# Performance work log

Hardware: AMD Instinct MI355X
Metric: run time of the kernel (lower is better)

The kernel has to match this reference:

```python
import jax, jax.numpy as jnp
import numpy as np

N, D, E, K = 8192, 1024, 16, 2
CAP = 1024  # capacity_per_expert


def setup_inputs() -> dict:
    key = jax.random.key(0)
    k1, k2, k3 = jax.random.split(key, 3)
    return {
        "moe_inp": jax.random.normal(k1, (N, D), dtype=jnp.float32),
        "gate_w": jax.random.normal(k2, (D, E), dtype=jnp.float32) * 0.02,
        "gate_b": jnp.zeros((E,), dtype=jnp.float32),
        "expert_w": jax.random.normal(k3, (E, D, D), dtype=jnp.float32) * 0.02,
        "expert_b": jnp.zeros((E, D), dtype=jnp.float32),
    }


def _capacity_keep_mask(expert_id, slot_score, num_experts, capacity):
    """For each flattened (token, k) slot assigned to an expert, keep only the
    `capacity` slots with the highest token score (gate_score.max over k),
    matching the argsort-based drop in _fmoe_limited_global_forward."""
    nslots = expert_id.shape[0]
    # sort slots by (expert asc, score desc)
    order = jnp.lexsort((-slot_score, expert_id))
    counts = jnp.bincount(expert_id, length=num_experts)
    starts = jnp.concatenate([jnp.zeros((1,), counts.dtype), jnp.cumsum(counts)[:-1]])
    pos_in_expert = jnp.arange(nslots) - starts[expert_id[order]]
    keep_sorted = pos_in_expert < capacity
    return jnp.zeros((nslots,), dtype=bool).at[order].set(keep_sorted)


def reference(moe_inp, gate_w, gate_b, expert_w, expert_b):
    n, d = moe_inp.shape
    e = expert_w.shape[0]
    # NaiveGate: linear -> top-k -> softmax over the k selected logits
    logits = moe_inp @ gate_w + gate_b                       # [N, E]
    top_v, top_i = jax.lax.top_k(logits, K)                  # [N, K]
    gate_score = jax.nn.softmax(top_v, axis=-1)              # [N, K]

    expert_id = top_i.reshape(-1)                            # [N*K]
    token_id = jnp.arange(n * K) // K                        # [N*K]
    mask_scores = gate_score.max(axis=-1)                    # [N] per-token score
    slot_score = mask_scores[token_id]                       # [N*K]

    keep = _capacity_keep_mask(expert_id, slot_score, e, CAP).reshape(n, K)

    # expert forward: FMoELinear y = x @ W_e^T + b_e (dense over experts, then gather)
    all_out = jnp.einsum('nd,efd->nef', moe_inp, expert_w) + expert_b  # [N, E, D]
    y = jnp.take_along_axis(all_out, top_i[:, :, None], axis=1)        # [N, K, D]
    # dropped (over-capacity) slots pass the scattered input through unchanged
    y = jnp.where(keep[:, :, None], y, moe_inp[:, None, :])
    # combine: bmm(gate_score [N,1,K], y [N,K,D]) -> [N, D]
    return jnp.einsum('nk,nkd->nd', gate_score, y)
```

## Files before the change

kernel.cpp:

```cpp
#include <hip/hip_runtime.h>
#include <hip/hip_bf16.h>
#include <math.h>

#define N_TOK 8192
#define DIM   1024
#define NEXP  16
#define TOPK  2
#define CAPE  1024
#define NSLOT (N_TOK*TOPK)

typedef __attribute__((ext_vector_type(8))) short     short8;
typedef __attribute__((ext_vector_type(4))) float     floatx4;
typedef __attribute__((ext_vector_type(4))) unsigned short ushort4v;

__device__ __forceinline__ unsigned short f2bf(float f) {
    unsigned u = __float_as_uint(f);
    u += 0x7FFFu + ((u >> 16) & 1u);
    return (unsigned short)(u >> 16);
}

#define GLOAD_LDS16(g, l) __builtin_amdgcn_global_load_lds( \
    (const __attribute__((address_space(1))) unsigned int*)(g), \
    (__attribute__((address_space(3))) unsigned int*)(l), 16, 0, 0)

#define RAW_BARRIER() asm volatile("s_barrier" ::: "memory")

__global__ void gwt_kernel(const float* __restrict__ gw, float* __restrict__ gwT) {
    int i = blockIdx.x * 256 + threadIdx.x;
    if (i >= DIM * NEXP) return;
    int d = i >> 4, e = i & 15;
    gwT[e * DIM + d] = gw[i];
}

__global__ __launch_bounds__(256) void gate_kernel(
        const float* __restrict__ x,
        const float* __restrict__ gwT,
        const float* __restrict__ gb,
        int* __restrict__ slot_expert,
        unsigned long long* __restrict__ slot_key,
        float* __restrict__ slot_gate,
        unsigned short* __restrict__ Xb) {
    const int t    = blockIdx.x * 4 + (threadIdx.x >> 6);
    const int lane = threadIdx.x & 63;

    const floatx4* xr = (const floatx4*)(x + (size_t)t * DIM);
    ushort4v* Xb4 = (ushort4v*)Xb + (size_t)t * 256;
    floatx4 xv[4];
#pragma unroll
    for (int i = 0; i < 4; i++) {
        xv[i] = xr[lane + i * 64];
        ushort4v o;
        o[0] = f2bf(xv[i][0]); o[1] = f2bf(xv[i][1]);
        o[2] = f2bf(xv[i][2]); o[3] = f2bf(xv[i][3]);
        Xb4[lane + i * 64] = o;
    }

    float acc[NEXP];
#pragma unroll
    for (int e = 0; e < NEXP; e++) {
        const floatx4* wr = (const floatx4*)(gwT + (size_t)e * DIM);
        float a = 0.f;
#pragma unroll
        for (int i = 0; i < 4; i++) {
            floatx4 w = wr[lane + i * 64];
            a += xv[i][0]*w[0] + xv[i][1]*w[1] + xv[i][2]*w[2] + xv[i][3]*w[3];
        }
        acc[e] = a;
    }
#pragma unroll
    for (int off = 32; off > 0; off >>= 1) {
#pragma unroll
        for (int e = 0; e < NEXP; e++) acc[e] += __shfl_down(acc[e], off, 64);
    }
    if (lane == 0) {
        float v0 = -1e30f; int i0 = 0;
#pragma unroll
        for (int e = 0; e < NEXP; e++) {
            float v = acc[e] + gb[e];
            acc[e] = v;
            if (v > v0) { v0 = v; i0 = e; }
        }
        float v1 = -1e30f; int i1 = 0;
#pragma unroll
        for (int e = 0; e < NEXP; e++) {
            if (e != i0 && acc[e] > v1) { v1 = acc[e]; i1 = e; }
        }
        float e1 = expf(v1 - v0);
        float den = 1.f + e1;
        float g0 = 1.f / den;
        float g1 = e1 / den;
        unsigned sb = __float_as_uint(g0);
        int s0 = 2 * t, s1 = 2 * t + 1;
        slot_expert[s0] = i0; slot_expert[s1] = i1;
        slot_gate[s0]   = g0; slot_gate[s1]   = g1;
        unsigned long long hi = ((unsigned long long)sb) << 32;
        slot_key[s0] = hi | (unsigned)(0xFFFFFFFFu - (unsigned)s0);
        slot_key[s1] = hi | (unsigned)(0xFFFFFFFFu - (unsigned)s1);
    }
}

__global__ __launch_bounds__(256) void bucket_kernel(
        const int* __restrict__ slot_expert,
        const unsigned long long* __restrict__ slot_key,
        int* __restrict__ counts,
        unsigned long long* __restrict__ buckets) {
    __shared__ int lcnt[NEXP];
    __shared__ int lbase[NEXP];
    const int tid = threadIdx.x;
    const int s = blockIdx.x * 256 + tid;
    if (tid < NEXP) lcnt[tid] = 0;
    __syncthreads();
    const int e = slot_expert[s];
    const unsigned long long key = slot_key[s];
    const int lpos = atomicAdd(&lcnt[e], 1);
    __syncthreads();
    if (tid < NEXP) lbase[tid] = lcnt[tid] ? atomicAdd(&counts[tid], lcnt[tid]) : 0;
    __syncthreads();
    buckets[(size_t)e * NSLOT + lbase[e] + lpos] = key;
}

__global__ __launch_bounds__(256) void keep_wave_kernel(
        const int* __restrict__ slot_expert,
        const unsigned long long* __restrict__ slot_key,
        const int* __restrict__ counts,
        const unsigned long long* __restrict__ buckets,
        int* __restrict__ slot_keep) {
    const int wv   = threadIdx.x >> 6;
    const int lane = threadIdx.x & 63;
    const int s    = blockIdx.x * 4 + wv;
    const int e    = slot_expert[s];
    const int c    = counts[e];
    int kp = 1;
    if (c > CAPE) {
        const unsigned long long k = slot_key[s];
        const unsigned long long* bk = buckets + (size_t)e * NSLOT;
        int rank = 0;
        for (int i = lane; i < c; i += 64) rank += (bk[i] > k) ? 1 : 0;
#pragma unroll
        for (int off = 32; off > 0; off >>= 1) rank += __shfl_down(rank, off, 64);
        kp = (__shfl(rank, 0, 64) < CAPE) ? 1 : 0;
    }
    if (lane == 0) slot_keep[s] = kp;
}

__global__ __launch_bounds__(256) void compact_kernel(
        const int* __restrict__ slot_expert,
        const int* __restrict__ slot_keep,
        int* __restrict__ ecount,
        int* __restrict__ elist,
        int* __restrict__ slot_pos) {
    __shared__ int lcnt[NEXP];
    __shared__ int lbase[NEXP];
    const int tid = threadIdx.x;
    const int s = blockIdx.x * 256 + tid;
    if (tid < NEXP) lcnt[tid] = 0;
    __syncthreads();
    const int e  = slot_expert[s];
    const int kp = slot_keep[s];
    int lpos = 0;
    if (kp) lpos = atomicAdd(&lcnt[e], 1);
    __syncthreads();
    if (tid < NEXP) lbase[tid] = lcnt[tid] ? atomicAdd(&ecount[tid], lcnt[tid]) : 0;
    __syncthreads();
    if (kp) {
        int p = lbase[e] + lpos;
        elist[e * CAPE + p] = s;
        if (slot_pos) slot_pos[s] = e * CAPE + p;
    }
}

__global__ void base_kernel(const float* __restrict__ x,
                            const int* __restrict__ keep,
                            const float* __restrict__ gate,
                            float* __restrict__ out) {
    int i = blockIdx.x * blockDim.x + threadIdx.x;
    int t = i >> 8;
    float c = 0.f;
    if (!keep[2 * t])     c += gate[2 * t];
    if (!keep[2 * t + 1]) c += gate[2 * t + 1];
    floatx4 v = ((const floatx4*)x)[i];
    ((floatx4*)out)[i] = v * c;
}

__global__ void cvt_kernel(const float* __restrict__ src,
                           unsigned short* __restrict__ dst, int n4) {
    int i = blockIdx.x * blockDim.x + threadIdx.x;
    if (i >= n4) return;
    floatx4 v = ((const floatx4*)src)[i];
    ushort4v o;
    o[0] = f2bf(v[0]); o[1] = f2bf(v[1]); o[2] = f2bf(v[2]); o[3] = f2bf(v[3]);
    ((ushort4v*)dst)[i] = o;
}

template <bool STORE_YS>
__global__ __launch_bounds__(512, 4)
void moe_gemm(const unsigned short* __restrict__ Xb,
              const unsigned short* __restrict__ Wb,
              const float* __restrict__ eb,
              const int* __restrict__ elist,
              const int* __restrict__ ecount,
              const float* __restrict__ slot_gate,
              float* __restrict__ ys,
              float* __restrict__ out) {
    __shared__ unsigned short As[2][256 * 32];
    __shared__ unsigned short Bs[2][128 * 32];

    const int e  = blockIdx.z;
    const int ne = ecount[e];
    const int m0 = blockIdx.y * 256;
    if (m0 >= ne) return;
    const int n0   = blockIdx.x * 128;
    const int tid  = threadIdx.x;
    const int wv   = tid >> 6;
    const int lane = tid & 63;
    const int q    = lane >> 4;
    const int l15  = lane & 15;
    const int wm   = (wv >> 1) * 64;
    const int wn   = (wv & 1) * 64;

    const int srow = wv * 16 + (lane >> 2);
    const int jsrc = (lane & 3) ^ ((lane >> 3) & 3);
    const unsigned short* gA0;
    const unsigned short* gA1;
    {
        int m = m0 + srow;
        int slot = elist[e * CAPE + (m < ne ? m : 0)];
        gA0 = Xb + (size_t)(slot >> 1) * DIM + jsrc * 8;
        m = m0 + 128 + srow;
        slot = elist[e * CAPE + (m < ne ? m : 0)];
        gA1 = Xb + (size_t)(slot >> 1) * DIM + jsrc * 8;
    }
    const unsigned short* gB0 =
        Wb + (size_t)e * DIM * DIM + (size_t)(n0 + srow) * DIM + jsrc * 8;

#define STAGE(b, k0) do { \
    GLOAD_LDS16(gA0 + (k0), &As[b][(wv * 16) * 32]); \
    GLOAD_LDS16(gA1 + (k0), &As[b][(128 + wv * 16) * 32]); \
    GLOAD_LDS16(gB0 + (k0), &Bs[b][(wv * 16) * 32]); } while (0)

    STAGE(0, 0);
    STAGE(1, 32);

    const int swz  = (q ^ ((l15 >> 1) & 3)) * 8;
    const int aoff = (wm + l15) * 32 + swz;
    const int boff = (wn + l15) * 32 + swz;

    floatx4 acc[4][4] = {};
    short8 a[4], b[4];

    for (int t = 0; t < 32; t++) {
        const int cur = t & 1;
        if (t == 31) { asm volatile("s_waitcnt vmcnt(0)" ::: "memory"); }
        else         { asm volatile("s_waitcnt vmcnt(3)" ::: "memory"); }
        __builtin_amdgcn_sched_barrier(0);
        RAW_BARRIER();

        const unsigned short* A_ = &As[cur][0];
        const unsigned short* B_ = &Bs[cur][0];
#pragma unroll
        for (int fi = 0; fi < 4; fi++) a[fi] = *(const short8*)(A_ + aoff + fi * 512);
#pragma unroll
        for (int fj = 0; fj < 4; fj++) b[fj] = *(const short8*)(B_ + boff + fj * 512);

        __builtin_amdgcn_s_setprio(1);
#pragma unroll
        for (int fi = 0; fi < 4; fi++)
#pragma unroll
            for (int fj = 0; fj < 4; fj++)
                acc[fi][fj] = __builtin_amdgcn_mfma_f32_16x16x32_bf16(
                    a[fi], b[fj], acc[fi][fj], 0, 0, 0);
        __builtin_amdgcn_s_setprio(0);
        RAW_BARRIER();

        if (t + 2 < 32) STAGE(cur, (t + 2) * 32);
    }
#undef STAGE

    float ebv[4];
#pragma unroll
    for (int fj = 0; fj < 4; fj++)
        ebv[fj] = eb[e * DIM + n0 + wn + fj * 16 + l15];
#pragma unroll
    for (int fi = 0; fi < 4; fi++) {
        const int mrow = m0 + wm + fi * 16 + q * 4;
#pragma unroll
        for (int r = 0; r < 4; r++) {
            int m = mrow + r;
            if (m >= ne) continue;
            if (STORE_YS) {
                float* yrow = ys + ((size_t)e * CAPE + m) * DIM + n0 + wn;
#pragma unroll
                for (int fj = 0; fj < 4; fj++)
                    yrow[fj * 16 + l15] = acc[fi][fj][r] + ebv[fj];
            } else {
                int slot = elist[e * CAPE + m];
                int tok  = slot >> 1;
                float g  = slot_gate[slot];
                float* orow = out + (size_t)tok * DIM + n0 + wn;
#pragma unroll
                for (int fj = 0; fj < 4; fj++)
                    atomicAdd(orow + fj * 16 + l15, g * (acc[fi][fj][r] + ebv[fj]));
            }
        }
    }
}

__global__ void combine_kernel(const float* __restrict__ x,
                               const float* __restrict__ ys,
                               const int* __restrict__ keep,
                               const int* __restrict__ pos,
                               const float* __restrict__ gate,
                               float* __restrict__ out) {
    int i = blockIdx.x * 256 + threadIdx.x;
    int t = i >> 8;
    int c = i & 255;
    int s0 = 2 * t, s1 = s0 + 1;
    floatx4 xv = ((const floatx4*)x)[i];
    float g0 = gate[s0], g1 = gate[s1];
    floatx4 r;
    if (keep[s0]) {
        floatx4 y0 = ((const floatx4*)ys)[((size_t)pos[s0] << 8) + c];
        r = y0 * g0;
    } else r = xv * g0;
    if (keep[s1]) {
        floatx4 y1 = ((const floatx4*)ys)[((size_t)pos[s1] << 8) + c];
        r += y1 * g1;
    } else r += xv * g1;
    ((floatx4*)out)[i] = r;
}

extern "C" void kernel_launch(void* const* d_in, const int* in_sizes, int n_in,
                              void* d_out, int out_size, void* d_ws, size_t ws_size,
                              hipStream_t stream) {
    const float* x  = (const float*)d_in[0];
    const float* gw = (const float*)d_in[1];
    const float* gb = (const float*)d_in[2];
    const float* ew = (const float*)d_in[3];
    const float* eb = (const float*)d_in[4];
    float* out = (float*)d_out;

    char* ws = (char*)d_ws;
    int* counts      = (int*)(ws + 0);
    int* ecount      = (int*)(ws + 64);
    int* slot_expert = (int*)(ws + 256);
    int* slot_keep   = (int*)(ws + 65792);
    float* slot_gate = (float*)(ws + 131328);
    unsigned long long* slot_key = (unsigned long long*)(ws + 196864);
    unsigned long long* buckets  = (unsigned long long*)(ws + 327936);
    int* elist       = (int*)(ws + 2425088);
    float* gwT       = (float*)(ws + 2490624);
    unsigned short* Xb = (unsigned short*)(ws + 2556160);
    unsigned short* Wb = (unsigned short*)(ws + 19333376);
    int* slot_pos    = (int*)(ws + 52887808);
    int* ecount2     = (int*)(ws + 52953088);
    float* ys        = (float*)(ws + 52953344);
    const size_t WS_NEED_YS = 52953344ull + (size_t)NEXP * CAPE * DIM * 4;

    const bool ys_path = (ws_size >= WS_NEED_YS);
    (void)ecount2;

    hipMemsetAsync(ws, 0, 256, stream);

    gwt_kernel <<<64, 256, 0, stream>>>(gw, gwT);
    gate_kernel<<<N_TOK / 4, 256, 0, stream>>>(x, gwT, gb, slot_expert, slot_key,
                                               slot_gate, Xb);
    bucket_kernel<<<NSLOT / 256, 256, 0, stream>>>(slot_expert, slot_key, counts, buckets);
    keep_wave_kernel<<<NSLOT / 4, 256, 0, stream>>>(slot_expert, slot_key, counts,
                                                    buckets, slot_keep);
    compact_kernel<<<NSLOT / 256, 256, 0, stream>>>(slot_expert, slot_keep, ecount, elist,
                                                    ys_path ? slot_pos : nullptr);
    cvt_kernel<<<(NEXP * DIM * DIM / 4) / 256, 256, 0, stream>>>(ew, Wb, NEXP * DIM * DIM / 4);

    if (ys_path) {
        moe_gemm<true><<<dim3(8, 4, 16), 512, 0, stream>>>(Xb, Wb, eb, elist, ecount,
                                                           slot_gate, ys, out);
        combine_kernel<<<N_TOK, 256, 0, stream>>>(x, ys, slot_keep, slot_pos,
                                                  slot_gate, out);
    } else {
        base_kernel<<<(N_TOK * DIM / 4) / 256, 256, 0, stream>>>(x, slot_keep,
                                                                 slot_gate, out);
        moe_gemm<false><<<dim3(8, 4, 16), 512, 0, stream>>>(Xb, Wb, eb, elist, ecount,
                                                            slot_gate, nullptr, out);
    }
}
```

Measured before the change: 243.8 us.

## Split MoE GEMM into per-k passes writing output directly, drop ys buffer

```diff
diff --git a/kernel.cpp b/kernel.cpp
--- a/kernel.cpp
+++ b/kernel.cpp
@@ -120,11 +120,14 @@
 }
 
 __global__ __launch_bounds__(256) void keep_wave_kernel(
+        const float* __restrict__ x,
         const int* __restrict__ slot_expert,
         const unsigned long long* __restrict__ slot_key,
         const int* __restrict__ counts,
         const unsigned long long* __restrict__ buckets,
-        int* __restrict__ slot_keep) {
+        const float* __restrict__ slot_gate,
+        int* __restrict__ slot_keep,
+        float* __restrict__ out) {
     const int wv   = threadIdx.x >> 6;
     const int lane = threadIdx.x & 63;
     const int s    = blockIdx.x * 4 + wv;
@@ -141,45 +144,49 @@
         kp = (__shfl(rank, 0, 64) < CAPE) ? 1 : 0;
     }
     if (lane == 0) slot_keep[s] = kp;
+    if (!kp && !(s & 1)) {
+        const int t = s >> 1;
+        const float g = slot_gate[s];
+        const floatx4* xr = (const floatx4*)(x + (size_t)t * DIM);
+        floatx4* orow = (floatx4*)(out + (size_t)t * DIM);
+#pragma unroll
+        for (int i = 0; i < 4; i++) orow[lane + i * 64] = xr[lane + i * 64] * g;
+    }
 }
 
 __global__ __launch_bounds__(256) void compact_kernel(
         const int* __restrict__ slot_expert,
         const int* __restrict__ slot_keep,
-        int* __restrict__ ecount,
-        int* __restrict__ elist,
-        int* __restrict__ slot_pos) {
-    __shared__ int lcnt[NEXP];
-    __shared__ int lbase[NEXP];
+        int* __restrict__ ecntP,
+        int* __restrict__ ndrop,
+        int* __restrict__ elist0,
+        int* __restrict__ elist1,
+        int* __restrict__ droplist) {
+    __shared__ int lcnt[2 * NEXP];
+    __shared__ int lbase[2 * NEXP];
+    __shared__ int ldc, ldbase;
     const int tid = threadIdx.x;
     const int s = blockIdx.x * 256 + tid;
-    if (tid < NEXP) lcnt[tid] = 0;
+    if (tid < 2 * NEXP) lcnt[tid] = 0;
+    if (tid == 2 * NEXP) ldc = 0;
     __syncthreads();
     const int e  = slot_expert[s];
+    const int p  = s & 1;
     const int kp = slot_keep[s];
-    int lpos = 0;
-    if (kp) lpos = atomicAdd(&lcnt[e], 1);
-    __syncthreads();
-    if (tid < NEXP) lbase[tid] = lcnt[tid] ? atomicAdd(&ecount[tid], lcnt[tid]) : 0;
+    const int idx = p * NEXP + e;
+    int lpos = 0, dpos = 0;
+    if (kp) lpos = atomicAdd(&lcnt[idx], 1);
+    else if (p) dpos = atomicAdd(&ldc, 1);
+    __syncthreads();
+    if (tid < 2 * NEXP) lbase[tid] = lcnt[tid] ? atomicAdd(&ecntP[tid], lcnt[tid]) : 0;
+    if (tid == 2 * NEXP) ldbase = ldc ? atomicAdd(ndrop, ldc) : 0;
     __syncthreads();
     if (kp) {
-        int p = lbase[e] + lpos;
-        elist[e * CAPE + p] = s;
-        if (slot_pos) slot_pos[s] = e * CAPE + p;
-    }
-}
-
-__global__ void base_kernel(const float* __restrict__ x,
-                            const int* __restrict__ keep,
-                            const float* __restrict__ gate,
-                            float* __restrict__ out) {
-    int i = blockIdx.x * blockDim.x + threadIdx.x;
-    int t = i >> 8;
-    float c = 0.f;
-    if (!keep[2 * t])     c += gate[2 * t];
-    if (!keep[2 * t + 1]) c += gate[2 * t + 1];
-    floatx4 v = ((const floatx4*)x)[i];
-    ((floatx4*)out)[i] = v * c;
+        int* el = p ? elist1 : elist0;
+        el[e * CAPE + lbase[idx] + lpos] = s;
+    } else if (p) {
+        droplist[ldbase + dpos] = s;
+    }
 }
 
 __global__ void cvt_kernel(const float* __restrict__ src,
@@ -192,21 +199,41 @@
     ((ushort4v*)dst)[i] = o;
 }
 
-template <bool STORE_YS>
+__global__ __launch_bounds__(256) void drop_add_kernel(
+        const float* __restrict__ x,
+        const float* __restrict__ slot_gate,
+        const int* __restrict__ droplist,
+        const int* __restrict__ ndrop,
+        float* __restrict__ out) {
+    const int wv   = blockIdx.x * 4 + (threadIdx.x >> 6);
+    const int lane = threadIdx.x & 63;
+    const int nw   = gridDim.x * 4;
+    const int nd   = *ndrop;
+    for (int i = wv; i < nd; i += nw) {
+        const int s = droplist[i];
+        const int t = s >> 1;
+        const float g = slot_gate[s];
+        const floatx4* xr = (const floatx4*)(x + (size_t)t * DIM);
+        floatx4* orow = (floatx4*)(out + (size_t)t * DIM);
+#pragma unroll
+        for (int j = 0; j < 4; j++) orow[lane + j * 64] += xr[lane + j * 64] * g;
+    }
+}
+
+template <int PASS>
 __global__ __launch_bounds__(512, 4)
 void moe_gemm(const unsigned short* __restrict__ Xb,
               const unsigned short* __restrict__ Wb,
               const float* __restrict__ eb,
               const int* __restrict__ elist,
-              const int* __restrict__ ecount,
+              const int* __restrict__ ecnt,
               const float* __restrict__ slot_gate,
-              float* __restrict__ ys,
               float* __restrict__ out) {
     __shared__ unsigned short As[2][256 * 32];
     __shared__ unsigned short Bs[2][128 * 32];
 
     const int e  = blockIdx.z;
-    const int ne = ecount[e];
+    const int ne = ecnt[e];
     const int m0 = blockIdx.y * 256;
     if (m0 >= ne) return;
     const int n0   = blockIdx.x * 128;
@@ -287,46 +314,18 @@
         for (int r = 0; r < 4; r++) {
             int m = mrow + r;
             if (m >= ne) continue;
-            if (STORE_YS) {
-                float* yrow = ys + ((size_t)e * CAPE + m) * DIM + n0 + wn;
-#pragma unroll
-                for (int fj = 0; fj < 4; fj++)
-                    yrow[fj * 16 + l15] = acc[fi][fj][r] + ebv[fj];
-            } else {
-                int slot = elist[e * CAPE + m];
-                int tok  = slot >> 1;
-                float g  = slot_gate[slot];
-                float* orow = out + (size_t)tok * DIM + n0 + wn;
-#pragma unroll
-                for (int fj = 0; fj < 4; fj++)
-                    atomicAdd(orow + fj * 16 + l15, g * (acc[fi][fj][r] + ebv[fj]));
+            int slot = elist[e * CAPE + m];
+            int tok  = slot >> 1;
+            float g  = slot_gate[slot];
+            float* orow = out + (size_t)tok * DIM + n0 + wn;
+#pragma unroll
+            for (int fj = 0; fj < 4; fj++) {
+                float v = g * (acc[fi][fj][r] + ebv[fj]);
+                if (PASS == 0) orow[fj * 16 + l15] = v;
+                else           orow[fj * 16 + l15] += v;
             }
         }
     }
-}
-
-__global__ void combine_kernel(const float* __restrict__ x,
-                               const float* __restrict__ ys,
-                               const int* __restrict__ keep,
-                               const int* __restrict__ pos,
-                               const float* __restrict__ gate,
-                               float* __restrict__ out) {
-    int i = blockIdx.x * 256 + threadIdx.x;
-    int t = i >> 8;
-    int c = i & 255;
-    int s0 = 2 * t, s1 = s0 + 1;
-    floatx4 xv = ((const floatx4*)x)[i];
-    float g0 = gate[s0], g1 = gate[s1];
-    floatx4 r;
-    if (keep[s0]) {
-        floatx4 y0 = ((const floatx4*)ys)[((size_t)pos[s0] << 8) + c];
-        r = y0 * g0;
-    } else r = xv * g0;
-    if (keep[s1]) {
-        floatx4 y1 = ((const floatx4*)ys)[((size_t)pos[s1] << 8) + c];
-        r += y1 * g1;
-    } else r += xv * g1;
-    ((floatx4*)out)[i] = r;
 }
 
 extern "C" void kernel_launch(void* const* d_in, const int* in_sizes, int n_in,
@@ -341,23 +340,19 @@
 
     char* ws = (char*)d_ws;
     int* counts      = (int*)(ws + 0);
-    int* ecount      = (int*)(ws + 64);
+    int* ecntP       = (int*)(ws + 64);
+    int* ndrop       = (int*)(ws + 192);
     int* slot_expert = (int*)(ws + 256);
     int* slot_keep   = (int*)(ws + 65792);
     float* slot_gate = (float*)(ws + 131328);
     unsigned long long* slot_key = (unsigned long long*)(ws + 196864);
     unsigned long long* buckets  = (unsigned long long*)(ws + 327936);
-    int* elist       = (int*)(ws + 2425088);
+    int* droplist    = (int*)(ws + 327936);
+    int* elist0      = (int*)(ws + 2425088);
     float* gwT       = (float*)(ws + 2490624);
     unsigned short* Xb = (unsigned short*)(ws + 2556160);
     unsigned short* Wb = (unsigned short*)(ws + 19333376);
-    int* slot_pos    = (int*)(ws + 52887808);
-    int* ecount2     = (int*)(ws + 52953088);
-    float* ys        = (float*)(ws + 52953344);
-    const size_t WS_NEED_YS = 52953344ull + (size_t)NEXP * CAPE * DIM * 4;
-
-    const bool ys_path = (ws_size >= WS_NEED_YS);
-    (void)ecount2;
+    int* elist1      = (int*)(ws + 52887808);
 
     hipMemsetAsync(ws, 0, 256, stream);
 
@@ -365,21 +360,15 @@
     gate_kernel<<<N_TOK / 4, 256, 0, stream>>>(x, gwT, gb, slot_expert, slot_key,
                                                slot_gate, Xb);
     bucket_kernel<<<NSLOT / 256, 256, 0, stream>>>(slot_expert, slot_key, counts, buckets);
-    keep_wave_kernel<<<NSLOT / 4, 256, 0, stream>>>(slot_expert, slot_key, counts,
-                                                    buckets, slot_keep);
-    compact_kernel<<<NSLOT / 256, 256, 0, stream>>>(slot_expert, slot_keep, ecount, elist,
-                                                    ys_path ? slot_pos : nullptr);
+    keep_wave_kernel<<<NSLOT / 4, 256, 0, stream>>>(x, slot_expert, slot_key, counts,
+                                                    buckets, slot_gate, slot_keep, out);
+    compact_kernel<<<NSLOT / 256, 256, 0, stream>>>(slot_expert, slot_keep, ecntP, ndrop,
+                                                    elist0, elist1, droplist);
     cvt_kernel<<<(NEXP * DIM * DIM / 4) / 256, 256, 0, stream>>>(ew, Wb, NEXP * DIM * DIM / 4);
 
-    if (ys_path) {
-        moe_gemm<true><<<dim3(8, 4, 16), 512, 0, stream>>>(Xb, Wb, eb, elist, ecount,
-                                                           slot_gate, ys, out);
-        combine_kernel<<<N_TOK, 256, 0, stream>>>(x, ys, slot_keep, slot_pos,
-                                                  slot_gate, out);
-    } else {
-        base_kernel<<<(N_TOK * DIM / 4) / 256, 256, 0, stream>>>(x, slot_keep,
-                                                                 slot_gate, out);
-        moe_gemm<false><<<dim3(8, 4, 16), 512, 0, stream>>>(Xb, Wb, eb, elist, ecount,
-                                                            slot_gate, nullptr, out);
-    }
-}
+    moe_gemm<0><<<dim3(8, 4, 16), 512, 0, stream>>>(Xb, Wb, eb, elist0, ecntP,
+                                                    slot_gate, out);
+    drop_add_kernel<<<64, 256, 0, stream>>>(x, slot_gate, droplist, ndrop, out);
+    moe_gemm<1><<<dim3(8, 4, 16), 512, 0, stream>>>(Xb, Wb, eb, elist1, ecntP + NEXP,
+                                                    slot_gate, out);
+}
```

Result: slower. 273.4 us (+12.1%).

## Fuse expert weight bf16 conversion into GEMM B-tile staging via registers

Applied to the files above, without the earlier changes.

```diff
diff --git a/kernel.cpp b/kernel.cpp
--- a/kernel.cpp
+++ b/kernel.cpp
@@ -182,20 +182,10 @@
     ((floatx4*)out)[i] = v * c;
 }
 
-__global__ void cvt_kernel(const float* __restrict__ src,
-                           unsigned short* __restrict__ dst, int n4) {
-    int i = blockIdx.x * blockDim.x + threadIdx.x;
-    if (i >= n4) return;
-    floatx4 v = ((const floatx4*)src)[i];
-    ushort4v o;
-    o[0] = f2bf(v[0]); o[1] = f2bf(v[1]); o[2] = f2bf(v[2]); o[3] = f2bf(v[3]);
-    ((ushort4v*)dst)[i] = o;
-}
-
 template <bool STORE_YS>
 __global__ __launch_bounds__(512, 4)
 void moe_gemm(const unsigned short* __restrict__ Xb,
-              const unsigned short* __restrict__ Wb,
+              const float* __restrict__ ew,
               const float* __restrict__ eb,
               const int* __restrict__ elist,
               const int* __restrict__ ecount,
@@ -230,16 +220,36 @@
         slot = elist[e * CAPE + (m < ne ? m : 0)];
         gA1 = Xb + (size_t)(slot >> 1) * DIM + jsrc * 8;
     }
-    const unsigned short* gB0 =
-        Wb + (size_t)e * DIM * DIM + (size_t)(n0 + srow) * DIM + jsrc * 8;
-
-#define STAGE(b, k0) do { \
+
+    const int brow = tid >> 2;
+    const int bj   = tid & 3;
+    const float* gBsrc =
+        ew + (size_t)e * DIM * DIM + (size_t)(n0 + brow) * DIM + bj * 8;
+    const int bdst = brow * 32 + (bj ^ ((brow >> 1) & 3)) * 8;
+
+#define STAGE_A(b, k0) do { \
     GLOAD_LDS16(gA0 + (k0), &As[b][(wv * 16) * 32]); \
-    GLOAD_LDS16(gA1 + (k0), &As[b][(128 + wv * 16) * 32]); \
-    GLOAD_LDS16(gB0 + (k0), &Bs[b][(wv * 16) * 32]); } while (0)
-
-    STAGE(0, 0);
-    STAGE(1, 32);
+    GLOAD_LDS16(gA1 + (k0), &As[b][(128 + wv * 16) * 32]); } while (0)
+
+    floatx4 bv0, bv1;
+#define LOADB(k0) do { bv0 = *(const floatx4*)(gBsrc + (k0)); \
+                       bv1 = *(const floatx4*)(gBsrc + (k0) + 4); } while (0)
+#define WRITEB(b) do { short8 t_; \
+    t_[0] = (short)f2bf(bv0[0]); t_[1] = (short)f2bf(bv0[1]); \
+    t_[2] = (short)f2bf(bv0[2]); t_[3] = (short)f2bf(bv0[3]); \
+    t_[4] = (short)f2bf(bv1[0]); t_[5] = (short)f2bf(bv1[1]); \
+    t_[6] = (short)f2bf(bv1[2]); t_[7] = (short)f2bf(bv1[3]); \
+    *(short8*)&Bs[b][bdst] = t_; } while (0)
+
+    LOADB(0);
+    STAGE_A(0, 0);
+    STAGE_A(1, 32);
+    asm volatile("s_waitcnt vmcnt(4)" ::: "memory");
+    __builtin_amdgcn_sched_barrier(0);
+    WRITEB(0);
+    LOADB(32);
+    asm volatile("s_waitcnt vmcnt(4)" ::: "memory");
+    __builtin_amdgcn_sched_barrier(0);
 
     const int swz  = (q ^ ((l15 >> 1) & 3)) * 8;
     const int aoff = (wm + l15) * 32 + swz;
@@ -250,8 +260,7 @@
 
     for (int t = 0; t < 32; t++) {
         const int cur = t & 1;
-        if (t == 31) { asm volatile("s_waitcnt vmcnt(0)" ::: "memory"); }
-        else         { asm volatile("s_waitcnt vmcnt(3)" ::: "memory"); }
+        asm volatile("s_waitcnt lgkmcnt(0)" ::: "memory");
         __builtin_amdgcn_sched_barrier(0);
         RAW_BARRIER();
 
@@ -272,9 +281,21 @@
         __builtin_amdgcn_s_setprio(0);
         RAW_BARRIER();
 
-        if (t + 2 < 32) STAGE(cur, (t + 2) * 32);
-    }
-#undef STAGE
+        if (t + 2 < 32) {
+            STAGE_A(cur, (t + 2) * 32);
+            asm volatile("s_waitcnt vmcnt(2)" ::: "memory");
+        } else {
+            asm volatile("s_waitcnt vmcnt(0)" ::: "memory");
+        }
+        __builtin_amdgcn_sched_barrier(0);
+        if (t + 1 < 32) {
+            WRITEB(cur ^ 1);
+            if (t + 2 < 32) LOADB((t + 2) * 32);
+        }
+    }
+#undef STAGE_A
+#undef LOADB
+#undef WRITEB
 
     float ebv[4];
 #pragma unroll
@@ -315,14 +336,16 @@
     int t = i >> 8;
     int c = i & 255;
     int s0 = 2 * t, s1 = s0 + 1;
-    floatx4 xv = ((const floatx4*)x)[i];
+    int k0 = keep[s0], k1 = keep[s1];
     float g0 = gate[s0], g1 = gate[s1];
+    floatx4 xv = {};
+    if (!k0 || !k1) xv = ((const floatx4*)x)[i];
     floatx4 r;
-    if (keep[s0]) {
+    if (k0) {
         floatx4 y0 = ((const floatx4*)ys)[((size_t)pos[s0] << 8) + c];
         r = y0 * g0;
     } else r = xv * g0;
-    if (keep[s1]) {
+    if (k1) {
         floatx4 y1 = ((const floatx4*)ys)[((size_t)pos[s1] << 8) + c];
         r += y1 * g1;
     } else r += xv * g1;
@@ -350,14 +373,11 @@
     int* elist       = (int*)(ws + 2425088);
     float* gwT       = (float*)(ws + 2490624);
     unsigned short* Xb = (unsigned short*)(ws + 2556160);
-    unsigned short* Wb = (unsigned short*)(ws + 19333376);
     int* slot_pos    = (int*)(ws + 52887808);
-    int* ecount2     = (int*)(ws + 52953088);
     float* ys        = (float*)(ws + 52953344);
     const size_t WS_NEED_YS = 52953344ull + (size_t)NEXP * CAPE * DIM * 4;
 
     const bool ys_path = (ws_size >= WS_NEED_YS);
-    (void)ecount2;
 
     hipMemsetAsync(ws, 0, 256, stream);
 
@@ -369,17 +389,16 @@
                                                     buckets, slot_keep);
     compact_kernel<<<NSLOT / 256, 256, 0, stream>>>(slot_expert, slot_keep, ecount, elist,
                                                     ys_path ? slot_pos : nullptr);
-    cvt_kernel<<<(NEXP * DIM * DIM / 4) / 256, 256, 0, stream>>>(ew, Wb, NEXP * DIM * DIM / 4);
 
     if (ys_path) {
-        moe_gemm<true><<<dim3(8, 4, 16), 512, 0, stream>>>(Xb, Wb, eb, elist, ecount,
+        moe_gemm<true><<<dim3(8, 4, 16), 512, 0, stream>>>(Xb, ew, eb, elist, ecount,
                                                            slot_gate, ys, out);
         combine_kernel<<<N_TOK, 256, 0, stream>>>(x, ys, slot_keep, slot_pos,
                                                   slot_gate, out);
     } else {
         base_kernel<<<(N_TOK * DIM / 4) / 256, 256, 0, stream>>>(x, slot_keep,
                                                                  slot_gate, out);
-        moe_gemm<false><<<dim3(8, 4, 16), 512, 0, stream>>>(Xb, Wb, eb, elist, ecount,
+        moe_gemm<false><<<dim3(8, 4, 16), 512, 0, stream>>>(Xb, ew, eb, elist, ecount,
                                                             slot_gate, nullptr, out);
     }
 }
```

After: 246.7 us. About the same (+1.2%).

## Fuse routing kernels and weight conversion, drop memset and redundant compact pass

Applied to the files above, without the earlier changes.

```diff
diff --git a/kernel.cpp b/kernel.cpp
--- a/kernel.cpp
+++ b/kernel.cpp
@@ -25,11 +25,21 @@
 
 #define RAW_BARRIER() asm volatile("s_barrier" ::: "memory")
 
-__global__ void gwt_kernel(const float* __restrict__ gw, float* __restrict__ gwT) {
-    int i = blockIdx.x * 256 + threadIdx.x;
-    if (i >= DIM * NEXP) return;
-    int d = i >> 4, e = i & 15;
-    gwT[e * DIM + d] = gw[i];
+__global__ void cvt_gwt_zero_kernel(const float* __restrict__ ew,
+                                    unsigned short* __restrict__ Wb,
+                                    const float* __restrict__ gw,
+                                    float* __restrict__ gwT,
+                                    int* __restrict__ zws) {
+    const int i = blockIdx.x * 256 + threadIdx.x;
+    if (blockIdx.x == 0 && threadIdx.x < 64) zws[threadIdx.x] = 0;
+    if (i < DIM * NEXP) {
+        int d = i >> 4, e = i & 15;
+        gwT[e * DIM + d] = gw[i];
+    }
+    floatx4 v = ((const floatx4*)ew)[i];
+    ushort4v o;
+    o[0] = f2bf(v[0]); o[1] = f2bf(v[1]); o[2] = f2bf(v[2]); o[3] = f2bf(v[3]);
+    ((ushort4v*)Wb)[i] = o;
 }
 
 __global__ __launch_bounds__(256) void gate_kernel(
@@ -39,9 +49,18 @@
         int* __restrict__ slot_expert,
         unsigned long long* __restrict__ slot_key,
         float* __restrict__ slot_gate,
-        unsigned short* __restrict__ Xb) {
-    const int t    = blockIdx.x * 4 + (threadIdx.x >> 6);
-    const int lane = threadIdx.x & 63;
+        unsigned short* __restrict__ Xb,
+        int* __restrict__ counts,
+        unsigned long long* __restrict__ buckets,
+        int* __restrict__ slot_bpos) {
+    __shared__ int se[8];
+    __shared__ unsigned long long sk[8];
+    __shared__ int lcnt[NEXP], lbase[NEXP], lpo[8];
+    const int tid  = threadIdx.x;
+    const int wv   = tid >> 6;
+    const int t    = blockIdx.x * 4 + wv;
+    const int lane = tid & 63;
+    if (tid < NEXP) lcnt[tid] = 0;
 
     const floatx4* xr = (const floatx4*)(x + (size_t)t * DIM);
     ushort4v* Xb4 = (ushort4v*)Xb + (size_t)t * 256;
@@ -94,78 +113,59 @@
         slot_expert[s0] = i0; slot_expert[s1] = i1;
         slot_gate[s0]   = g0; slot_gate[s1]   = g1;
         unsigned long long hi = ((unsigned long long)sb) << 32;
-        slot_key[s0] = hi | (unsigned)(0xFFFFFFFFu - (unsigned)s0);
-        slot_key[s1] = hi | (unsigned)(0xFFFFFFFFu - (unsigned)s1);
-    }
-}
-
-__global__ __launch_bounds__(256) void bucket_kernel(
-        const int* __restrict__ slot_expert,
-        const unsigned long long* __restrict__ slot_key,
-        int* __restrict__ counts,
-        unsigned long long* __restrict__ buckets) {
-    __shared__ int lcnt[NEXP];
-    __shared__ int lbase[NEXP];
-    const int tid = threadIdx.x;
-    const int s = blockIdx.x * 256 + tid;
-    if (tid < NEXP) lcnt[tid] = 0;
+        unsigned long long k0 = hi | (unsigned)(0xFFFFFFFFu - (unsigned)s0);
+        unsigned long long k1 = hi | (unsigned)(0xFFFFFFFFu - (unsigned)s1);
+        slot_key[s0] = k0; slot_key[s1] = k1;
+        se[2 * wv] = i0; se[2 * wv + 1] = i1;
+        sk[2 * wv] = k0; sk[2 * wv + 1] = k1;
+    }
     __syncthreads();
-    const int e = slot_expert[s];
-    const unsigned long long key = slot_key[s];
-    const int lpos = atomicAdd(&lcnt[e], 1);
+    if (tid < 8) lpo[tid] = atomicAdd(&lcnt[se[tid]], 1);
     __syncthreads();
     if (tid < NEXP) lbase[tid] = lcnt[tid] ? atomicAdd(&counts[tid], lcnt[tid]) : 0;
     __syncthreads();
-    buckets[(size_t)e * NSLOT + lbase[e] + lpos] = key;
-}
-
-__global__ __launch_bounds__(256) void keep_wave_kernel(
+    if (tid < 8) {
+        int e = se[tid];
+        int p = lbase[e] + lpo[tid];
+        buckets[(size_t)e * NSLOT + p] = sk[tid];
+        slot_bpos[blockIdx.x * 8 + tid] = p;
+    }
+}
+
+__global__ __launch_bounds__(256) void keep_compact_kernel(
         const int* __restrict__ slot_expert,
         const unsigned long long* __restrict__ slot_key,
         const int* __restrict__ counts,
         const unsigned long long* __restrict__ buckets,
-        int* __restrict__ slot_keep) {
+        int* __restrict__ slot_keep,
+        int* __restrict__ elist,
+        int* __restrict__ slot_pos) {
     const int wv   = threadIdx.x >> 6;
     const int lane = threadIdx.x & 63;
     const int s    = blockIdx.x * 4 + wv;
     const int e    = slot_expert[s];
     const int c    = counts[e];
-    int kp = 1;
-    if (c > CAPE) {
+    int kp = 1, pos;
+    if (c <= CAPE) {
+        pos = slot_keep[s];
+    } else {
         const unsigned long long k = slot_key[s];
         const unsigned long long* bk = buckets + (size_t)e * NSLOT;
         int rank = 0;
         for (int i = lane; i < c; i += 64) rank += (bk[i] > k) ? 1 : 0;
 #pragma unroll
         for (int off = 32; off > 0; off >>= 1) rank += __shfl_down(rank, off, 64);
-        kp = (__shfl(rank, 0, 64) < CAPE) ? 1 : 0;
-    }
-    if (lane == 0) slot_keep[s] = kp;
-}
-
-__global__ __launch_bounds__(256) void compact_kernel(
-        const int* __restrict__ slot_expert,
-        const int* __restrict__ slot_keep,
-        int* __restrict__ ecount,
-        int* __restrict__ elist,
-        int* __restrict__ slot_pos) {
-    __shared__ int lcnt[NEXP];
-    __shared__ int lbase[NEXP];
-    const int tid = threadIdx.x;
-    const int s = blockIdx.x * 256 + tid;
-    if (tid < NEXP) lcnt[tid] = 0;
-    __syncthreads();
-    const int e  = slot_expert[s];
-    const int kp = slot_keep[s];
-    int lpos = 0;
-    if (kp) lpos = atomicAdd(&lcnt[e], 1);
-    __syncthreads();
-    if (tid < NEXP) lbase[tid] = lcnt[tid] ? atomicAdd(&ecount[tid], lcnt[tid]) : 0;
-    __syncthreads();
-    if (kp) {
-        int p = lbase[e] + lpos;
-        elist[e * CAPE + p] = s;
-        if (slot_pos) slot_pos[s] = e * CAPE + p;
+        rank = __shfl(rank, 0, 64);
+        kp  = (rank < CAPE) ? 1 : 0;
+        pos = rank;
+    }
+    if (lane == 0) {
+        slot_keep[s] = kp;
+        if (kp) {
+            int p = e * CAPE + pos;
+            elist[p]    = s;
+            slot_pos[s] = p;
+        }
     }
 }
 
@@ -182,23 +182,13 @@
     ((floatx4*)out)[i] = v * c;
 }
 
-__global__ void cvt_kernel(const float* __restrict__ src,
-                           unsigned short* __restrict__ dst, int n4) {
-    int i = blockIdx.x * blockDim.x + threadIdx.x;
-    if (i >= n4) return;
-    floatx4 v = ((const floatx4*)src)[i];
-    ushort4v o;
-    o[0] = f2bf(v[0]); o[1] = f2bf(v[1]); o[2] = f2bf(v[2]); o[3] = f2bf(v[3]);
-    ((ushort4v*)dst)[i] = o;
-}
-
 template <bool STORE_YS>
 __global__ __launch_bounds__(512, 4)
 void moe_gemm(const unsigned short* __restrict__ Xb,
               const unsigned short* __restrict__ Wb,
               const float* __restrict__ eb,
               const int* __restrict__ elist,
-              const int* __restrict__ ecount,
+              const int* __restrict__ counts,
               const float* __restrict__ slot_gate,
               float* __restrict__ ys,
               float* __restrict__ out) {
@@ -206,7 +196,7 @@
     __shared__ unsigned short Bs[2][128 * 32];
 
     const int e  = blockIdx.z;
-    const int ne = ecount[e];
+    int ne = counts[e]; if (ne > CAPE) ne = CAPE;
     const int m0 = blockIdx.y * 256;
     if (m0 >= ne) return;
     const int n0   = blockIdx.x * 128;
@@ -315,14 +305,16 @@
     int t = i >> 8;
     int c = i & 255;
     int s0 = 2 * t, s1 = s0 + 1;
-    floatx4 xv = ((const floatx4*)x)[i];
+    int k0 = keep[s0], k1 = keep[s1];
     float g0 = gate[s0], g1 = gate[s1];
+    floatx4 xv = {};
+    if (!k0 || !k1) xv = ((const floatx4*)x)[i];
     floatx4 r;
-    if (keep[s0]) {
+    if (k0) {
         floatx4 y0 = ((const floatx4*)ys)[((size_t)pos[s0] << 8) + c];
         r = y0 * g0;
     } else r = xv * g0;
-    if (keep[s1]) {
+    if (k1) {
         floatx4 y1 = ((const floatx4*)ys)[((size_t)pos[s1] << 8) + c];
         r += y1 * g1;
     } else r += xv * g1;
@@ -341,7 +333,6 @@
 
     char* ws = (char*)d_ws;
     int* counts      = (int*)(ws + 0);
-    int* ecount      = (int*)(ws + 64);
     int* slot_expert = (int*)(ws + 256);
     int* slot_keep   = (int*)(ws + 65792);
     float* slot_gate = (float*)(ws + 131328);
@@ -352,34 +343,29 @@
     unsigned short* Xb = (unsigned short*)(ws + 2556160);
     unsigned short* Wb = (unsigned short*)(ws + 19333376);
     int* slot_pos    = (int*)(ws + 52887808);
-    int* ecount2     = (int*)(ws + 52953088);
     float* ys        = (float*)(ws + 52953344);
     const size_t WS_NEED_YS = 52953344ull + (size_t)NEXP * CAPE * DIM * 4;
 
     const bool ys_path = (ws_size >= WS_NEED_YS);
-    (void)ecount2;
-
-    hipMemsetAsync(ws, 0, 256, stream);
-
-    gwt_kernel <<<64, 256, 0, stream>>>(gw, gwT);
+
+    cvt_gwt_zero_kernel<<<(NEXP * DIM * DIM / 4) / 256, 256, 0, stream>>>(
+        ew, Wb, gw, gwT, (int*)ws);
     gate_kernel<<<N_TOK / 4, 256, 0, stream>>>(x, gwT, gb, slot_expert, slot_key,
-                                               slot_gate, Xb);
-    bucket_kernel<<<NSLOT / 256, 256, 0, stream>>>(slot_expert, slot_key, counts, buckets);
-    keep_wave_kernel<<<NSLOT / 4, 256, 0, stream>>>(slot_expert, slot_key, counts,
-                                                    buckets, slot_keep);
-    compact_kernel<<<NSLOT / 256, 256, 0, stream>>>(slot_expert, slot_keep, ecount, elist,
-                                                    ys_path ? slot_pos : nullptr);
-    cvt_kernel<<<(NEXP * DIM * DIM / 4) / 256, 256, 0, stream>>>(ew, Wb, NEXP * DIM * DIM / 4);
+                                               slot_gate, Xb, counts, buckets,
+                                               slot_keep);
+    keep_compact_kernel<<<NSLOT / 4, 256, 0, stream>>>(slot_expert, slot_key, counts,
+                                                       buckets, slot_keep, elist,
+                                                       slot_pos);
 
     if (ys_path) {
-        moe_gemm<true><<<dim3(8, 4, 16), 512, 0, stream>>>(Xb, Wb, eb, elist, ecount,
+        moe_gemm<true><<<dim3(8, 4, 16), 512, 0, stream>>>(Xb, Wb, eb, elist, counts,
                                                            slot_gate, ys, out);
         combine_kernel<<<N_TOK, 256, 0, stream>>>(x, ys, slot_keep, slot_pos,
                                                   slot_gate, out);
     } else {
         base_kernel<<<(N_TOK * DIM / 4) / 256, 256, 0, stream>>>(x, slot_keep,
                                                                  slot_gate, out);
-        moe_gemm<false><<<dim3(8, 4, 16), 512, 0, stream>>>(Xb, Wb, eb, elist, ecount,
+        moe_gemm<false><<<dim3(8, 4, 16), 512, 0, stream>>>(Xb, Wb, eb, elist, counts,
                                                             slot_gate, nullptr, out);
     }
 }
```

After: 246.0 us. About the same (+0.9%).
